# Kernel tuning notes

Hardware: AMD Instinct MI355X
Metric: run time of the kernel (lower is better)

The kernel has to match this reference:

```python
import jax, jax.numpy as jnp
import numpy as np

N, E = 50000, 800000
IN, EIN, HID, OUT = 128, 64, 64, 64
NEG_SLOPE = 0.2


def setup_inputs() -> dict:
    key = jax.random.key(0)
    ks = jax.random.split(key, 24)
    p = lambda k, shape: jax.random.normal(k, shape, jnp.float32) * 0.05
    return {
        'x': jax.random.normal(ks[0], (N, IN), jnp.float32),
        'edge_index': jax.random.randint(ks[1], (2, E), 0, N, jnp.int64),
        'edge_attr': jax.random.normal(ks[2], (E, EIN), jnp.float32),
        'batch': jnp.sort(jax.random.randint(ks[3], (N,), 0, 64, jnp.int64)),
        # GATConv 1 (in -> hidden, edge_dim=EIN)
        'W1': p(ks[4], (IN, HID)), 'a_src1': p(ks[5], (HID,)), 'a_dst1': p(ks[6], (HID,)),
        'We1': p(ks[7], (EIN, HID)), 'a_e1': p(ks[8], (HID,)), 'b1': jnp.zeros((HID,), jnp.float32),
        # GATConv 2 (hidden -> out)
        'W2': p(ks[9], (HID, OUT)), 'a_src2': p(ks[10], (OUT,)), 'a_dst2': p(ks[11], (OUT,)),
        'We2': p(ks[12], (EIN, OUT)), 'a_e2': p(ks[13], (OUT,)), 'b2': jnp.zeros((OUT,), jnp.float32),
        # edge MLP
        'Wm1': p(ks[14], (EIN, HID)), 'bm1': jnp.zeros((HID,), jnp.float32),
        'Wm2': p(ks[15], (HID, OUT)), 'bm2': jnp.zeros((OUT,), jnp.float32),
    }


def _gat(x, src, dst, edge_attr, W, a_s, a_d, We, a_e, b, n):
    # PyG GATConv (heads=1): add self-loops with edge_attr fill_value='mean'
    ones = jnp.ones((src.shape[0],), x.dtype)
    deg = jax.ops.segment_sum(ones, dst, num_segments=n)
    loop_attr = jax.ops.segment_sum(edge_attr, dst, num_segments=n) / jnp.maximum(deg, 1.0)[:, None]
    ar = jnp.arange(n)
    src2 = jnp.concatenate([src, ar])
    dst2 = jnp.concatenate([dst, ar])
    ea = jnp.concatenate([edge_attr, loop_attr], axis=0)  # [E+N, EIN]
    h = x @ W                                             # [N, C]
    a_src = h @ a_s                                       # [N]
    a_dst = h @ a_d                                       # [N]
    a_edge = (ea @ We) @ a_e                              # [E+N]
    alpha = jax.nn.leaky_relu(a_src[src2] + a_dst[dst2] + a_edge, NEG_SLOPE)
    # scatter-softmax over incoming edges of each dst node
    amax = jax.ops.segment_max(alpha, dst2, num_segments=n)
    ex = jnp.exp(alpha - amax[dst2])
    denom = jax.ops.segment_sum(ex, dst2, num_segments=n)
    coef = ex / denom[dst2]                               # [E+N]
    out = jax.ops.segment_sum(h[src2] * coef[:, None], dst2, num_segments=n)
    return out + b


def reference(x, edge_index, edge_attr, batch,
              W1, a_src1, a_dst1, We1, a_e1, b1,
              W2, a_src2, a_dst2, We2, a_e2, b2,
              Wm1, bm1, Wm2, bm2):
    n = x.shape[0]
    src, dst = edge_index[0], edge_index[1]
    h = _gat(x, src, dst, edge_attr, W1, a_src1, a_dst1, We1, a_e1, b1, n)
    h = jax.nn.elu(h)
    h = _gat(h, src, dst, edge_attr, W2, a_src2, a_dst2, We2, a_e2, b2, n)
    e = jax.nn.relu(edge_attr @ Wm1 + bm1) @ Wm2 + bm2
    return h, e, batch
```

## Files before the change

### kernel.cpp

```cpp
#include <hip/hip_runtime.h>

constexpr int NN = 50000;
constexpr int NE = 800000;
constexpr int C = 64;
constexpr int IN_DIM = 128;
constexpr float NEG = 0.2f;
constexpr int NB = (NN + 255) / 256;
constexpr int FEATB = (NN + 127) / 128;

typedef __attribute__((ext_vector_type(8))) short short8;
typedef __attribute__((ext_vector_type(4))) float f32x4;

__device__ __forceinline__ unsigned short f2bf(float f) {
    unsigned u = __float_as_uint(f);
    unsigned r = 0x7FFFu + ((u >> 16) & 1u);
    return (unsigned short)((u + r) >> 16);
}
__device__ __forceinline__ unsigned pack_bf2(float a, float b) {
    return (unsigned)f2bf(a) | ((unsigned)f2bf(b) << 16);
}
__device__ __forceinline__ float bf2f(unsigned u) {
    return __uint_as_float(u << 16);
}

__global__ __launch_bounds__(256) void k_setup(
        const float* __restrict__ We1, const float* __restrict__ ae1v,
        const float* __restrict__ We2, const float* __restrict__ ae2v,
        const float* __restrict__ W1, const float* __restrict__ as1,
        const float* __restrict__ ad1,
        const float* __restrict__ W2, const float* __restrict__ as2,
        const float* __restrict__ ad2,
        const int* __restrict__ batch,
        float* __restrict__ vecs, int* __restrict__ hist, int* __restrict__ bagg,
        float* __restrict__ out_b) {
    int t = blockIdx.x * 256 + threadIdx.x;
    if (t < 512) {
        const float* M; const float* v; int row;
        if      (t < 64)  { M = We1; v = ae1v; row = t; }
        else if (t < 128) { M = We2; v = ae2v; row = t - 64; }
        else if (t < 256) { M = W1;  v = as1;  row = t - 128; }
        else if (t < 384) { M = W1;  v = ad1;  row = t - 256; }
        else if (t < 448) { M = W2;  v = as2;  row = t - 384; }
        else              { M = W2;  v = ad2;  row = t - 448; }
        float s = 0.f;
        #pragma unroll
        for (int c = 0; c < 64; ++c) s += M[row * 64 + c] * v[c];
        vecs[t] = s;
    }
    if (t < NN) { hist[t] = 0; out_b[t] = (float)batch[t]; }
    if (t < NB) bagg[t] = 0;
}

__device__ __forceinline__ void mlp_body(char* __restrict__ LDSB, int bid,
        const float* __restrict__ ea, const int* __restrict__ dst,
        const float* __restrict__ Wm1, const float* __restrict__ bm1,
        const float* __restrict__ Wm2, const float* __restrict__ bm2,
        const float* __restrict__ wv,
        float* __restrict__ eout, float* __restrict__ ae1, float* __restrict__ ae2,
        int* __restrict__ hist) {
    constexpr int AP = 144;
    char* Atile = LDSB;
    char* Bt1 = LDSB + 128 * AP;
    char* Bt2 = Bt1 + 64 * AP;
    const int t = threadIdx.x;
    const long long E0 = (long long)bid * 128;
    const int l = t & 63;

    if (t < 128) atomicAdd(&hist[dst[E0 + t]], 1);

    {
        const int j = t & 15;
        const int eb = t >> 4;
        float4 wk1 = *(const float4*)&wv[j * 4];
        float4 wk2 = *(const float4*)&wv[64 + j * 4];
        const f32x4* g = (const f32x4*)(ea + E0 * 64);
        float s1[8], s2[8];
        #pragma unroll
        for (int q = 0; q < 8; ++q) {
            f32x4 v = __builtin_nontemporal_load(&g[t + 256 * q]);
            int e = eb + 16 * q;
            s1[q] = v[0] * wk1.x + v[1] * wk1.y + v[2] * wk1.z + v[3] * wk1.w;
            s2[q] = v[0] * wk2.x + v[1] * wk2.y + v[2] * wk2.z + v[3] * wk2.w;
            uint2 wr;
            wr.x = pack_bf2(v[0], v[1]);
            wr.y = pack_bf2(v[2], v[3]);
            *(uint2*)(Atile + e * AP + j * 8) = wr;
        }
        #pragma unroll
        for (int off = 1; off < 16; off <<= 1) {
            #pragma unroll
            for (int q = 0; q < 8; ++q) {
                s1[q] += __shfl_xor(s1[q], off);
                s2[q] += __shfl_xor(s2[q], off);
            }
        }
        float o1 = 0.f, o2 = 0.f;
        #pragma unroll
        for (int q = 0; q < 8; ++q) {
            if (j == q)     o1 = s1[q];
            if (j == q + 8) o2 = s2[q];
        }
        if (j < 8) ae1[E0 + eb + 16 * j] = o1;
        else       ae2[E0 + eb + 16 * (j - 8)] = o2;
    }
    {
        const int c = t & 63, kq = t >> 6;
        #pragma unroll
        for (int i = 0; i < 16; i += 2) {
            int k = kq * 16 + i;
            *(unsigned*)(Bt1 + c * AP + k * 2) = pack_bf2(Wm1[k * 64 + c], Wm1[(k + 1) * 64 + c]);
            *(unsigned*)(Bt2 + c * AP + k * 2) = pack_bf2(Wm2[k * 64 + c], Wm2[(k + 1) * 64 + c]);
        }
    }
    __syncthreads();

    const int m0 = (t >> 6) * 32;
    const int lr = l & 15;
    const int lq = l >> 4;
    const int lk = lq * 8;

    f32x4 acc[4][2] = {};
    #pragma unroll
    for (int ks = 0; ks < 2; ++ks) {
        int ko = ks * 32 + lk;
        short8 a0 = *(const short8*)(Atile + (m0 + lr) * AP + ko * 2);
        short8 a1 = *(const short8*)(Atile + (m0 + 16 + lr) * AP + ko * 2);
        #pragma unroll
        for (int ct = 0; ct < 4; ++ct) {
            short8 b = *(const short8*)(Bt1 + (ct * 16 + lr) * AP + ko * 2);
            acc[ct][0] = __builtin_amdgcn_mfma_f32_16x16x32_bf16(b, a0, acc[ct][0], 0, 0, 0);
            acc[ct][1] = __builtin_amdgcn_mfma_f32_16x16x32_bf16(b, a1, acc[ct][1], 0, 0, 0);
        }
    }
    #pragma unroll
    for (int ct = 0; ct < 4; ++ct) {
        float4 bv = *(const float4*)&bm1[ct * 16 + lq * 4];
        #pragma unroll
        for (int et = 0; et < 2; ++et) {
            float v0 = fmaxf(acc[ct][et][0] + bv.x, 0.f);
            float v1 = fmaxf(acc[ct][et][1] + bv.y, 0.f);
            float v2 = fmaxf(acc[ct][et][2] + bv.z, 0.f);
            float v3 = fmaxf(acc[ct][et][3] + bv.w, 0.f);
            uint2 w;
            w.x = pack_bf2(v0, v1);
            w.y = pack_bf2(v2, v3);
            int e = m0 + et * 16 + lr;
            *(uint2*)(Atile + e * AP + (ct * 16 + lq * 4) * 2) = w;
        }
    }
    f32x4 acc2[4][2] = {};
    #pragma unroll
    for (int ks = 0; ks < 2; ++ks) {
        int ko = ks * 32 + lk;
        short8 a0 = *(const short8*)(Atile + (m0 + lr) * AP + ko * 2);
        short8 a1 = *(const short8*)(Atile + (m0 + 16 + lr) * AP + ko * 2);
        #pragma unroll
        for (int ct = 0; ct < 4; ++ct) {
            short8 b = *(const short8*)(Bt2 + (ct * 16 + lr) * AP + ko * 2);
            acc2[ct][0] = __builtin_amdgcn_mfma_f32_16x16x32_bf16(b, a0, acc2[ct][0], 0, 0, 0);
            acc2[ct][1] = __builtin_amdgcn_mfma_f32_16x16x32_bf16(b, a1, acc2[ct][1], 0, 0, 0);
        }
    }
    #pragma unroll
    for (int ct = 0; ct < 4; ++ct) {
        float4 bv = *(const float4*)&bm2[ct * 16 + lq * 4];
        #pragma unroll
        for (int et = 0; et < 2; ++et) {
            int e = m0 + et * 16 + lr;
            float4 o;
            o.x = acc2[ct][et][0] + bv.x;
            o.y = acc2[ct][et][1] + bv.y;
            o.z = acc2[ct][et][2] + bv.z;
            o.w = acc2[ct][et][3] + bv.w;
            *(float4*)&eout[(E0 + e) * 64 + ct * 16 + lq * 4] = o;
        }
    }
}

template <int K, bool BF16IN>
__device__ __forceinline__ void feat_body(char* __restrict__ LDSB, int bid,
        const void* __restrict__ xv, const float* __restrict__ W,
        const float* __restrict__ uv,
        unsigned short* __restrict__ h, float* __restrict__ asrc,
        float* __restrict__ adst, int M) {
    constexpr int AP = K * 2 + 16;
    constexpr int QW = K / 4;
    constexpr int NQ = K / 8;
    constexpr int EPQ = 256 / QW;
    char* Atile = LDSB;
    char* Bt = LDSB + 128 * AP;
    const int t = threadIdx.x;
    const int M0 = bid * 128;
    const int l = t & 63;

    {
        const int j = t % QW;
        const int eb = t / QW;
        float4 wk1 = *(const float4*)&uv[j * 4];
        float4 wk2 = *(const float4*)&uv[K + j * 4];
        float s1[NQ], s2[NQ];
        #pragma unroll
        for (int q = 0; q < NQ; ++q) {
            int e = eb + EPQ * q;
            float v0, v1, v2, v3;
            uint2 wr;
            if constexpr (BF16IN) {
                const uint2* g = (const uint2*)xv + (long long)M0 * (K / 4);
                uint2 w = make_uint2(0u, 0u);
                if (M0 + e < M) w = g[t + 256 * q];
                v0 = bf2f(w.x & 0xFFFFu); v1 = bf2f(w.x >> 16);
                v2 = bf2f(w.y & 0xFFFFu); v3 = bf2f(w.y >> 16);
                wr = w;
            } else {
                const float4* g = (const float4*)xv + (long long)M0 * (K / 4);
                float4 v = make_float4(0.f, 0.f, 0.f, 0.f);
                if (M0 + e < M) v = g[t + 256 * q];
                v0 = v.x; v1 = v.y; v2 = v.z; v3 = v.w;
                wr.x = pack_bf2(v.x, v.y);
                wr.y = pack_bf2(v.z, v.w);
            }
            s1[q] = v0 * wk1.x + v1 * wk1.y + v2 * wk1.z + v3 * wk1.w;
            s2[q] = v0 * wk2.x + v1 * wk2.y + v2 * wk2.z + v3 * wk2.w;
            *(uint2*)(Atile + e * AP + j * 8) = wr;
        }
        #pragma unroll
        for (int off = 1; off < QW; off <<= 1) {
            #pragma unroll
            for (int q = 0; q < NQ; ++q) {
                s1[q] += __shfl_xor(s1[q], off);
                s2[q] += __shfl_xor(s2[q], off);
            }
        }
        float o1 = 0.f, o2 = 0.f;
        #pragma unroll
        for (int q = 0; q < NQ; ++q) {
            if (j == q)      o1 = s1[q];
            if (j == q + NQ) o2 = s2[q];
        }
        if (j < NQ) { int e = eb + EPQ * j;        if (M0 + e < M) asrc[M0 + e] = o1; }
        else        { int e = eb + EPQ * (j - NQ); if (M0 + e < M) adst[M0 + e] = o2; }
    }
    {
        const int c = t & 63, kq = t >> 6;
        #pragma unroll
        for (int i = 0; i < K / 4; i += 2) {
            int k = kq * (K / 4) + i;
            *(unsigned*)(Bt + c * AP + k * 2) = pack_bf2(W[k * 64 + c], W[(k + 1) * 64 + c]);
        }
    }
    __syncthreads();

    const int m0 = (t >> 6) * 32;
    const int lr = l & 15;
    const int lq = l >> 4;
    const int lk = lq * 8;

    f32x4 acc[4][2] = {};
    #pragma unroll
    for (int ks = 0; ks < K / 32; ++ks) {
        int ko = ks * 32 + lk;
        short8 a0 = *(const short8*)(Atile + (m0 + lr) * AP + ko * 2);
        short8 a1 = *(const short8*)(Atile + (m0 + 16 + lr) * AP + ko * 2);
        #pragma unroll
        for (int ct = 0; ct < 4; ++ct) {
            short8 b = *(const short8*)(Bt + (ct * 16 + lr) * AP + ko * 2);
            acc[ct][0] = __builtin_amdgcn_mfma_f32_16x16x32_bf16(b, a0, acc[ct][0], 0, 0, 0);
            acc[ct][1] = __builtin_amdgcn_mfma_f32_16x16x32_bf16(b, a1, acc[ct][1], 0, 0, 0);
        }
    }
    #pragma unroll
    for (int ct = 0; ct < 4; ++ct)
    #pragma unroll
    for (int et = 0; et < 2; ++et) {
        int row = m0 + et * 16 + lr;
        if (M0 + row < M) {
            uint2 w;
            w.x = pack_bf2(acc[ct][et][0], acc[ct][et][1]);
            w.y = pack_bf2(acc[ct][et][2], acc[ct][et][3]);
            *(uint2*)&h[(long long)(M0 + row) * 64 + ct * 16 + lq * 4] = w;
        }
    }
}

__global__ __launch_bounds__(256) void k_mlp_feat(
        const float* __restrict__ ea, const int* __restrict__ dst,
        const float* __restrict__ Wm1, const float* __restrict__ bm1,
        const float* __restrict__ Wm2, const float* __restrict__ bm2,
        const float* __restrict__ wv,
        float* __restrict__ eout, float* __restrict__ ae1, float* __restrict__ ae2,
        int* __restrict__ hist,
        const float* __restrict__ x, const float* __restrict__ W1,
        const float* __restrict__ uv,
        unsigned short* __restrict__ h, float* __restrict__ asrc,
        float* __restrict__ adst) {
    __shared__ char LDSB[128 * (IN_DIM * 2 + 16) + 64 * (IN_DIM * 2 + 16)];
    if (blockIdx.x < FEATB) {
        feat_body<IN_DIM, false>(LDSB, blockIdx.x, x, W1, uv, h, asrc, adst, NN);
    } else {
        mlp_body(LDSB, blockIdx.x - FEATB, ea, dst, Wm1, bm1, Wm2, bm2, wv,
                 eout, ae1, ae2, hist);
    }
}

__global__ __launch_bounds__(256) void k_feat2(
        const void* __restrict__ xv, const float* __restrict__ W,
        const float* __restrict__ uv,
        unsigned short* __restrict__ h, float* __restrict__ asrc,
        float* __restrict__ adst) {
    __shared__ char LDSB[128 * 144 + 64 * 144];
    feat_body<C, true>(LDSB, blockIdx.x, xv, W, uv, h, asrc, adst, NN);
}

__global__ __launch_bounds__(256) void k_scan_f(const int* __restrict__ hist,
        int* __restrict__ row_ptr, int* __restrict__ cursor, int* __restrict__ bagg) {
    __shared__ int s[256];
    __shared__ int red[5];
    const int t = threadIdx.x, b = blockIdx.x;
    const int idx = b * 256 + t;
    int v = (idx < NN) ? hist[idx] : 0;
    s[t] = v;
    __syncthreads();
    #pragma unroll
    for (int off = 1; off < 256; off <<= 1) {
        int x = (t >= off) ? s[t - off] : 0;
        __syncthreads();
        s[t] += x;
        __syncthreads();
    }
    if (t == 255)
        __hip_atomic_store(&bagg[b], (s[255] << 1) | 1,
                           __ATOMIC_RELEASE, __HIP_MEMORY_SCOPE_AGENT);
    int contrib = 0;
    if (t < b) {
        int a;
        do {
            a = __hip_atomic_load(&bagg[t], __ATOMIC_ACQUIRE, __HIP_MEMORY_SCOPE_AGENT);
        } while (!(a & 1));
        contrib = a >> 1;
    }
    #pragma unroll
    for (int off = 32; off; off >>= 1) contrib += __shfl_down(contrib, off);
    if ((t & 63) == 0) red[t >> 6] = contrib;
    __syncthreads();
    if (t == 0) red[4] = red[0] + red[1] + red[2] + red[3];
    __syncthreads();
    int offset = red[4];
    if (idx < NN) {
        int rp = offset + s[t] - v;
        row_ptr[idx] = rp;
        cursor[idx] = rp;
    }
    if (idx == NN) row_ptr[NN] = NE;
}

__global__ void k_scatter(const int* __restrict__ src, const int* __restrict__ dst,
                          const float* __restrict__ ae1, const float* __restrict__ ae2,
                          int* __restrict__ cursor, uint2* __restrict__ csr) {
    int t = blockIdx.x * blockDim.x + threadIdx.x;
    if (t >= NE) return;
    int d = dst[t];
    int pos = atomicAdd(&cursor[d], 1);
    csr[pos] = make_uint2((unsigned)src[t], pack_bf2(ae1[t], ae2[t]));
}

template <bool IS_L1>
__global__ void k_gat(const int* __restrict__ row_ptr, const uint2* __restrict__ csr,
                      const float* __restrict__ asrc, const float* __restrict__ adst,
                      const unsigned short* __restrict__ h, const float* __restrict__ bias,
                      void* __restrict__ outv) {
    int n = blockIdx.x * 4 + (threadIdx.x >> 6);
    if (n >= NN) return;
    int lane = threadIdx.x & 63;
    int g = lane >> 4, s = lane & 15;
    int beg = row_ptr[n], end = row_ptr[n + 1];
    float adn = adst[n];
    float m = -1e30f, l = 0.f, sum_ae = 0.f;
    float4 acc = make_float4(0.f, 0.f, 0.f, 0.f);

    int i = beg + g;
    uint2 rc = make_uint2(0u, 0u);
    ushort4 hu = make_ushort4(0, 0, 0, 0);
    float asv = 0.f;
    if (i < end) {
        rc = csr[i];
        hu = *(const ushort4*)&h[(long long)rc.x * 64 + s * 4];
        asv = asrc[rc.x];
    }
    for (; i < end; i += 4) {
        uint2 rn = rc; ushort4 hn = hu; float asn = asv;
        if (i + 4 < end) {
            rn = csr[i + 4];
            hn = *(const ushort4*)&h[(long long)rn.x * 64 + s * 4];
            asn = asrc[rn.x];
        }
        float ae = IS_L1 ? bf2f(rc.y & 0xFFFFu) : bf2f(rc.y >> 16);
        sum_ae += ae;
        float a = asv + adn + ae;
        a = a > 0.f ? a : NEG * a;
        float mn = fmaxf(m, a);
        float sc = __expf(m - mn), p = __expf(a - mn);
        l = l * sc + p;
        acc.x = acc.x * sc + p * bf2f(hu.x);
        acc.y = acc.y * sc + p * bf2f(hu.y);
        acc.z = acc.z * sc + p * bf2f(hu.z);
        acc.w = acc.w * sc + p * bf2f(hu.w);
        m = mn;
        rc = rn; hu = hn; asv = asn;
    }
    #pragma unroll
    for (int off = 16; off < 64; off <<= 1) {
        float mo = __shfl_xor(m, off);
        float lo = __shfl_xor(l, off);
        float ax = __shfl_xor(acc.x, off);
        float ay = __shfl_xor(acc.y, off);
        float az = __shfl_xor(acc.z, off);
        float aw = __shfl_xor(acc.w, off);
        float so = __shfl_xor(sum_ae, off);
        float mn = fmaxf(m, mo);
        float s1 = __expf(m - mn), s2 = __expf(mo - mn);
        l = l * s1 + lo * s2;
        acc.x = acc.x * s1 + ax * s2;
        acc.y = acc.y * s1 + ay * s2;
        acc.z = acc.z * s1 + az * s2;
        acc.w = acc.w * s1 + aw * s2;
        sum_ae += so;
        m = mn;
    }
    {
        float deg = (float)(end - beg);
        float ae = sum_ae / fmaxf(deg, 1.f);
        float a = asrc[n] + adn + ae;
        a = a > 0.f ? a : NEG * a;
        ushort4 hun = *(const ushort4*)&h[(long long)n * 64 + s * 4];
        float mn = fmaxf(m, a);
        float sc = __expf(m - mn), p = __expf(a - mn);
        l = l * sc + p;
        acc.x = acc.x * sc + p * bf2f(hun.x);
        acc.y = acc.y * sc + p * bf2f(hun.y);
        acc.z = acc.z * sc + p * bf2f(hun.z);
        acc.w = acc.w * sc + p * bf2f(hun.w);
    }
    if (g == 0) {
        float4 o;
        o.x = acc.x / l + bias[s * 4 + 0];
        o.y = acc.y / l + bias[s * 4 + 1];
        o.z = acc.z / l + bias[s * 4 + 2];
        o.w = acc.w / l + bias[s * 4 + 3];
        if (IS_L1) {
            o.x = o.x > 0.f ? o.x : expm1f(o.x);
            o.y = o.y > 0.f ? o.y : expm1f(o.y);
            o.z = o.z > 0.f ? o.z : expm1f(o.z);
            o.w = o.w > 0.f ? o.w : expm1f(o.w);
            uint2 w;
            w.x = pack_bf2(o.x, o.y);
            w.y = pack_bf2(o.z, o.w);
            *(uint2*)&((unsigned short*)outv)[(long long)n * 64 + s * 4] = w;
        } else {
            *(float4*)&((float*)outv)[(long long)n * 64 + s * 4] = o;
        }
    }
}

extern "C" void kernel_launch(void* const* d_in, const int* in_sizes, int n_in,
                              void* d_out, int out_size, void* d_ws, size_t ws_size,
                              hipStream_t stream) {
    const float* x     = (const float*)d_in[0];
    const int*   eidx  = (const int*)d_in[1];
    const float* eattr = (const float*)d_in[2];
    const int*   batch = (const int*)d_in[3];
    const float* W1 = (const float*)d_in[4];
    const float* as1 = (const float*)d_in[5];
    const float* ad1 = (const float*)d_in[6];
    const float* We1 = (const float*)d_in[7];
    const float* vae1 = (const float*)d_in[8];
    const float* b1  = (const float*)d_in[9];
    const float* W2 = (const float*)d_in[10];
    const float* as2 = (const float*)d_in[11];
    const float* ad2 = (const float*)d_in[12];
    const float* We2 = (const float*)d_in[13];
    const float* vae2 = (const float*)d_in[14];
    const float* b2  = (const float*)d_in[15];
    const float* Wm1 = (const float*)d_in[16];
    const float* bm1 = (const float*)d_in[17];
    const float* Wm2 = (const float*)d_in[18];
    const float* bm2 = (const float*)d_in[19];

    const int* src = eidx;
    const int* dst = eidx + NE;

    float* out_h = (float*)d_out;
    float* out_e = out_h + (long long)NN * C;
    float* out_b = out_e + (long long)NE * C;

    uint2* csr    = (uint2*)d_ws;
    float* ae1    = (float*)(csr + NE);
    float* ae2    = ae1 + NE;
    unsigned short* out1b = (unsigned short*)(ae2 + NE);
    unsigned short* h = out1b + (long long)NN * C;
    float* asrc   = (float*)(h + (long long)NN * C);
    float* adst   = asrc + NN;
    float* vecs   = adst + NN;
    int*   hist   = (int*)(vecs + 512);
    int*   row_ptr= hist + NN;
    int*   cursor = row_ptr + NN + 1;
    int*   bagg   = cursor + NN;

    k_setup<<<NB, 256, 0, stream>>>(We1, vae1, We2, vae2, W1, as1, ad1,
                                    W2, as2, ad2, batch, vecs, hist, bagg, out_b);

    k_mlp_feat<<<FEATB + NE / 128, 256, 0, stream>>>(
        eattr, dst, Wm1, bm1, Wm2, bm2, vecs, out_e, ae1, ae2, hist,
        x, W1, vecs + 128, h, asrc, adst);

    k_scan_f<<<NB, 256, 0, stream>>>(hist, row_ptr, cursor, bagg);
    k_scatter<<<(NE + 255) / 256, 256, 0, stream>>>(src, dst, ae1, ae2, cursor, csr);

    k_gat<true><<<(NN + 3) / 4, 256, 0, stream>>>(row_ptr, csr, asrc, adst, h, b1, out1b);

    k_feat2<<<FEATB, 256, 0, stream>>>(out1b, W2, vecs + 384, h, asrc, adst);
    k_gat<false><<<(NN + 3) / 4, 256, 0, stream>>>(row_ptr, csr, asrc, adst, h, b2, out_h);
}
```

Before: 265.6 us.

## Fuse layer-2 feature transform into layer-1 GAT aggregation epilogue

Removes the separate k_feat2 kernel and computes h2 = elu(out1) @ W2 plus the src/dst attention scalars directly in the k_gat<true> epilogue. Each wave stages its node's output row in LDS and then computes one output channel per lane. This drops the bf16 intermediate round-trip through global memory and one kernel launch. In exchange the GEMM work moves from an MFMA tiled kernel to scalar per-lane dot products, with W2 read from cache by every wave, and it adds shared memory to k_gat.

```diff
diff --git a/kernel.cpp b/kernel.cpp
--- a/kernel.cpp
+++ b/kernel.cpp
@@ -177,9 +177,9 @@
     }
 }
 
-template <int K, bool BF16IN>
+template <int K>
 __device__ __forceinline__ void feat_body(char* __restrict__ LDSB, int bid,
-        const void* __restrict__ xv, const float* __restrict__ W,
+        const float* __restrict__ xv, const float* __restrict__ W,
         const float* __restrict__ uv,
         unsigned short* __restrict__ h, float* __restrict__ asrc,
         float* __restrict__ adst, int M) {
@@ -202,25 +202,14 @@
         #pragma unroll
         for (int q = 0; q < NQ; ++q) {
             int e = eb + EPQ * q;
-            float v0, v1, v2, v3;
+            const float4* g = (const float4*)xv + (long long)M0 * (K / 4);
+            float4 v = make_float4(0.f, 0.f, 0.f, 0.f);
+            if (M0 + e < M) v = g[t + 256 * q];
             uint2 wr;
-            if constexpr (BF16IN) {
-                const uint2* g = (const uint2*)xv + (long long)M0 * (K / 4);
-                uint2 w = make_uint2(0u, 0u);
-                if (M0 + e < M) w = g[t + 256 * q];
-                v0 = bf2f(w.x & 0xFFFFu); v1 = bf2f(w.x >> 16);
-                v2 = bf2f(w.y & 0xFFFFu); v3 = bf2f(w.y >> 16);
-                wr = w;
-            } else {
-                const float4* g = (const float4*)xv + (long long)M0 * (K / 4);
-                float4 v = make_float4(0.f, 0.f, 0.f, 0.f);
-                if (M0 + e < M) v = g[t + 256 * q];
-                v0 = v.x; v1 = v.y; v2 = v.z; v3 = v.w;
-                wr.x = pack_bf2(v.x, v.y);
-                wr.y = pack_bf2(v.z, v.w);
-            }
-            s1[q] = v0 * wk1.x + v1 * wk1.y + v2 * wk1.z + v3 * wk1.w;
-            s2[q] = v0 * wk2.x + v1 * wk2.y + v2 * wk2.z + v3 * wk2.w;
+            wr.x = pack_bf2(v.x, v.y);
+            wr.y = pack_bf2(v.z, v.w);
+            s1[q] = v.x * wk1.x + v.y * wk1.y + v.z * wk1.z + v.w * wk1.w;
+            s2[q] = v.x * wk2.x + v.y * wk2.y + v.z * wk2.z + v.w * wk2.w;
             *(uint2*)(Atile + e * AP + j * 8) = wr;
         }
         #pragma unroll
@@ -295,20 +284,11 @@
         float* __restrict__ adst) {
     __shared__ char LDSB[128 * (IN_DIM * 2 + 16) + 64 * (IN_DIM * 2 + 16)];
     if (blockIdx.x < FEATB) {
-        feat_body<IN_DIM, false>(LDSB, blockIdx.x, x, W1, uv, h, asrc, adst, NN);
+        feat_body<IN_DIM>(LDSB, blockIdx.x, x, W1, uv, h, asrc, adst, NN);
     } else {
         mlp_body(LDSB, blockIdx.x - FEATB, ea, dst, Wm1, bm1, Wm2, bm2, wv,
                  eout, ae1, ae2, hist);
     }
-}
-
-__global__ __launch_bounds__(256) void k_feat2(
-        const void* __restrict__ xv, const float* __restrict__ W,
-        const float* __restrict__ uv,
-        unsigned short* __restrict__ h, float* __restrict__ asrc,
-        float* __restrict__ adst) {
-    __shared__ char LDSB[128 * 144 + 64 * 144];
-    feat_body<C, true>(LDSB, blockIdx.x, xv, W, uv, h, asrc, adst, NN);
 }
 
 __global__ __launch_bounds__(256) void k_scan_f(const int* __restrict__ hist,
@@ -367,8 +347,12 @@
 __global__ void k_gat(const int* __restrict__ row_ptr, const uint2* __restrict__ csr,
                       const float* __restrict__ asrc, const float* __restrict__ adst,
                       const unsigned short* __restrict__ h, const float* __restrict__ bias,
-                      void* __restrict__ outv) {
-    int n = blockIdx.x * 4 + (threadIdx.x >> 6);
+                      const float* __restrict__ W2, const float* __restrict__ uv2,
+                      unsigned short* __restrict__ h2out, float* __restrict__ asrc2,
+                      float* __restrict__ adst2, float* __restrict__ outf) {
+    __shared__ float sh_o[4][64];
+    int wv = threadIdx.x >> 6;
+    int n = blockIdx.x * 4 + wv;
     if (n >= NN) return;
     int lane = threadIdx.x & 63;
     int g = lane >> 4, s = lane & 15;
@@ -440,23 +424,42 @@
         acc.z = acc.z * sc + p * bf2f(hun.z);
         acc.w = acc.w * sc + p * bf2f(hun.w);
     }
-    if (g == 0) {
-        float4 o;
-        o.x = acc.x / l + bias[s * 4 + 0];
-        o.y = acc.y / l + bias[s * 4 + 1];
-        o.z = acc.z / l + bias[s * 4 + 2];
-        o.w = acc.w / l + bias[s * 4 + 3];
-        if (IS_L1) {
+    if constexpr (IS_L1) {
+        if (g == 0) {
+            float4 o;
+            o.x = acc.x / l + bias[s * 4 + 0];
+            o.y = acc.y / l + bias[s * 4 + 1];
+            o.z = acc.z / l + bias[s * 4 + 2];
+            o.w = acc.w / l + bias[s * 4 + 3];
             o.x = o.x > 0.f ? o.x : expm1f(o.x);
             o.y = o.y > 0.f ? o.y : expm1f(o.y);
             o.z = o.z > 0.f ? o.z : expm1f(o.z);
             o.w = o.w > 0.f ? o.w : expm1f(o.w);
-            uint2 w;
-            w.x = pack_bf2(o.x, o.y);
-            w.y = pack_bf2(o.z, o.w);
-            *(uint2*)&((unsigned short*)outv)[(long long)n * 64 + s * 4] = w;
-        } else {
-            *(float4*)&((float*)outv)[(long long)n * 64 + s * 4] = o;
+            sh_o[wv][s * 4 + 0] = o.x;
+            sh_o[wv][s * 4 + 1] = o.y;
+            sh_o[wv][s * 4 + 2] = o.z;
+            sh_o[wv][s * 4 + 3] = o.w;
+        }
+        float h2 = 0.f;
+        #pragma unroll 8
+        for (int c = 0; c < 64; ++c)
+            h2 += sh_o[wv][c] * W2[c * 64 + lane];
+        float v1 = h2 * uv2[lane], v2 = h2 * uv2[64 + lane];
+        #pragma unroll
+        for (int off = 32; off; off >>= 1) {
+            v1 += __shfl_xor(v1, off);
+            v2 += __shfl_xor(v2, off);
+        }
+        if (lane == 0) { asrc2[n] = v1; adst2[n] = v2; }
+        h2out[(long long)n * 64 + lane] = f2bf(h2);
+    } else {
+        if (g == 0) {
+            float4 o;
+            o.x = acc.x / l + bias[s * 4 + 0];
+            o.y = acc.y / l + bias[s * 4 + 1];
+            o.z = acc.z / l + bias[s * 4 + 2];
+            o.w = acc.w / l + bias[s * 4 + 3];
+            *(float4*)&outf[(long long)n * 64 + s * 4] = o;
         }
     }
 }
@@ -495,11 +498,13 @@
     uint2* csr    = (uint2*)d_ws;
     float* ae1    = (float*)(csr + NE);
     float* ae2    = ae1 + NE;
-    unsigned short* out1b = (unsigned short*)(ae2 + NE);
-    unsigned short* h = out1b + (long long)NN * C;
+    unsigned short* h2 = (unsigned short*)(ae2 + NE);
+    unsigned short* h = h2 + (long long)NN * C;
     float* asrc   = (float*)(h + (long long)NN * C);
     float* adst   = asrc + NN;
-    float* vecs   = adst + NN;
+    float* asrc2  = adst + NN;
+    float* adst2  = asrc2 + NN;
+    float* vecs   = adst2 + NN;
     int*   hist   = (int*)(vecs + 512);
     int*   row_ptr= hist + NN;
     int*   cursor = row_ptr + NN + 1;
@@ -515,8 +520,11 @@
     k_scan_f<<<NB, 256, 0, stream>>>(hist, row_ptr, cursor, bagg);
     k_scatter<<<(NE + 255) / 256, 256, 0, stream>>>(src, dst, ae1, ae2, cursor, csr);
 
-    k_gat<true><<<(NN + 3) / 4, 256, 0, stream>>>(row_ptr, csr, asrc, adst, h, b1, out1b);
-
-    k_feat2<<<FEATB, 256, 0, stream>>>(out1b, W2, vecs + 384, h, asrc, adst);
-    k_gat<false><<<(NN + 3) / 4, 256, 0, stream>>>(row_ptr, csr, asrc, adst, h, b2, out_h);
-}
+    k_gat<true><<<(NN + 3) / 4, 256, 0, stream>>>(row_ptr, csr, asrc, adst, h, b1,
+                                                  W2, vecs + 384, h2, asrc2, adst2,
+                                                  nullptr);
+
+    k_gat<false><<<(NN + 3) / 4, 256, 0, stream>>>(row_ptr, csr, asrc2, adst2, h2, b2,
+                                                   nullptr, nullptr, nullptr, nullptr,
+                                                   nullptr, out_h);
+}
```

Measured after the change: 269.4 us. No clear change (+1.4%).
